# Optimization experiments

Hardware: AMD Instinct MI355X
Metric: run time of the kernel (lower is better)

Reference implementation:

```python
import jax, jax.numpy as jnp
import numpy as np

B, V, FN, C = 8, 50000, 100000, 64


def setup_inputs() -> dict:
    key = jax.random.key(0)
    keys = iter(jax.random.split(key, 16))
    inp = {}
    inp["centers"] = jax.random.normal(next(keys), (B, 3, FN), jnp.float32)
    inp["verts"] = jax.random.normal(next(keys), (B, V, 3), jnp.float32)
    inp["faces"] = jax.random.randint(next(keys), (B, FN, 3), 0, V)

    def bn(p):
        inp[p + "g"] = jnp.ones((C,), jnp.float32)
        inp[p + "bt"] = jnp.zeros((C,), jnp.float32)
        inp[p + "m"] = jnp.zeros((C,), jnp.float32)
        inp[p + "v"] = jnp.ones((C,), jnp.float32)

    inp["cw1"] = jax.random.normal(next(keys), (C, 3), jnp.float32) * 0.1
    inp["cb1"] = jnp.zeros((C,), jnp.float32); bn("c1")
    inp["cw2"] = jax.random.normal(next(keys), (C, C), jnp.float32) * 0.1
    inp["cb2"] = jnp.zeros((C,), jnp.float32); bn("c2")
    inp["vw1"] = jax.random.normal(next(keys), (C, 6), jnp.float32) * 0.1
    inp["vb1"] = jnp.zeros((C,), jnp.float32); bn("v1")
    inp["vw2"] = jax.random.normal(next(keys), (C, C), jnp.float32) * 0.1
    inp["vb2"] = jnp.zeros((C,), jnp.float32); bn("v2")
    inp["sw"] = jax.random.normal(next(keys), (C, 2 * C), jnp.float32) * 0.1
    inp["sb"] = jnp.zeros((C,), jnp.float32); bn("s1")
    return inp


def _cbr(x, w, b, g, bt, m, v, eps=1e-5):
    # 1x1 Conv1d == pointwise GEMM over channel dim, then eval-mode BN, then ReLU
    y = jnp.einsum('bcf,oc->bof', x, w) + b[:, None]
    y = (y - m[:, None]) * (g[:, None] / jnp.sqrt(v[:, None] + eps)) + bt[:, None]
    return jax.nn.relu(y)


def _forward(faces, centers, verts,
             cw1, cb1, c1g, c1bt, c1m, c1v, cw2, cb2, c2g, c2bt, c2m, c2v,
             vw1, vb1, v1g, v1bt, v1m, v1v, vw2, vb2, v2g, v2bt, v2m, v2v,
             sw, sb, s1g, s1bt, s1m, s1v):
    Bb, Fn, _ = faces.shape
    # gather 3 corner vertices per face: [B, 3F, 3] -> [B, 9, F] (v0xyz, v1xyz, v2xyz)
    idx = faces.reshape(Bb, Fn * 3)
    corners = jnp.take_along_axis(verts, idx[:, :, None], axis=1)
    c9 = corners.reshape(Bb, Fn, 9).transpose(0, 2, 1)

    def vmlp(x):
        return _cbr(_cbr(x, vw1, vb1, v1g, v1bt, v1m, v1v), vw2, vb2, v2g, v2bt, v2m, v2v)

    vfeat = (vmlp(c9[:, :6])
             + vmlp(c9[:, 3:9])
             + vmlp(jnp.concatenate([c9[:, 6:9], c9[:, :3]], axis=1))) / 3.0
    cfeat = _cbr(_cbr(centers, cw1, cb1, c1g, c1bt, c1m, c1v), cw2, cb2, c2g, c2bt, c2m, c2v)
    return _cbr(jnp.concatenate([cfeat, vfeat], axis=1), sw, sb, s1g, s1bt, s1m, s1v)


def reference(centers, verts, faces,
              cw1, cb1, c1g, c1bt, c1m, c1v, cw2, cb2, c2g, c2bt, c2m, c2v,
              vw1, vb1, v1g, v1bt, v1m, v1v, vw2, vb2, v2g, v2bt, v2m, v2v,
              sw, sb, s1g, s1bt, s1m, s1v):
    return _forward(faces, centers, verts,
                    cw1, cb1, c1g, c1bt, c1m, c1v, cw2, cb2, c2g, c2bt, c2m, c2v,
                    vw1, vb1, v1g, v1bt, v1m, v1v, vw2, vb2, v2g, v2bt, v2m, v2v,
                    sw, sb, s1g, s1bt, s1m, s1v)
```

## Files before the change

kernel.cpp:

```cpp
#include <hip/hip_runtime.h>
#include <cstddef>
#include <cstdint>

#define FN_ 100000
#define V_  50000
#define B_  8
#define NT  64
#define NBX ((FN_ + NT - 1) / NT)

#define WS_SHS 49152

typedef _Float16 f16;
typedef f16   f16x8 __attribute__((ext_vector_type(8)));
typedef float f32x4 __attribute__((ext_vector_type(4)));

struct Ptrs { const void* p[33]; };

union Pk8 { f16 h[8]; uint4 u; };

__device__ __forceinline__ uint32_t pack2(float a, float b) {
  return __builtin_bit_cast(uint32_t, __builtin_amdgcn_cvt_pkrtz(a, b));
}
__device__ __forceinline__ uint32_t pack_relu2(float a, float b) {
  uint32_t r, x = pack2(a, b);
  asm("v_pk_max_f16 %0, %1, 0" : "=v"(r) : "v"(x));
  return r;
}

__global__ __launch_bounds__(1024) void sd_prep(Ptrs in, f16* __restrict__ wsW,
                                                float* __restrict__ shsG)
{
  const float* __restrict__ cw1 = (const float*)in.p[3];
  const float* __restrict__ cb1 = (const float*)in.p[4];
  const float* __restrict__ c1g = (const float*)in.p[5];
  const float* __restrict__ c1bt= (const float*)in.p[6];
  const float* __restrict__ c1m = (const float*)in.p[7];
  const float* __restrict__ c1v = (const float*)in.p[8];
  const float* __restrict__ cw2 = (const float*)in.p[9];
  const float* __restrict__ cb2 = (const float*)in.p[10];
  const float* __restrict__ c2g = (const float*)in.p[11];
  const float* __restrict__ c2bt= (const float*)in.p[12];
  const float* __restrict__ c2m = (const float*)in.p[13];
  const float* __restrict__ c2v = (const float*)in.p[14];
  const float* __restrict__ vw1 = (const float*)in.p[15];
  const float* __restrict__ vb1 = (const float*)in.p[16];
  const float* __restrict__ v1g = (const float*)in.p[17];
  const float* __restrict__ v1bt= (const float*)in.p[18];
  const float* __restrict__ v1m = (const float*)in.p[19];
  const float* __restrict__ v1v = (const float*)in.p[20];
  const float* __restrict__ vw2 = (const float*)in.p[21];
  const float* __restrict__ vb2 = (const float*)in.p[22];
  const float* __restrict__ v2g = (const float*)in.p[23];
  const float* __restrict__ v2bt= (const float*)in.p[24];
  const float* __restrict__ v2m = (const float*)in.p[25];
  const float* __restrict__ v2v = (const float*)in.p[26];
  const float* __restrict__ sw  = (const float*)in.p[27];
  const float* __restrict__ sb  = (const float*)in.p[28];
  const float* __restrict__ s1g = (const float*)in.p[29];
  const float* __restrict__ s1bt= (const float*)in.p[30];
  const float* __restrict__ s1m = (const float*)in.p[31];
  const float* __restrict__ s1v = (const float*)in.p[32];

  __shared__ float scsL[448];
  const int tid = threadIdx.x;

  if (tid < 448) {
    const float *g, *v, *bb, *m, *bt; int o; float mul = 1.f;
    if (tid < 64)       { o = tid;      g=c1g; v=c1v; bb=cb1; m=c1m; bt=c1bt; }
    else if (tid < 256) { o = tid & 63; g=v1g; v=v1v; bb=vb1; m=v1m; bt=v1bt; }
    else if (tid < 320) { o = tid-256;  g=c2g; v=c2v; bb=cb2; m=c2m; bt=c2bt; }
    else if (tid < 384) { o = tid-320;  g=v2g; v=v2v; bb=vb2; m=v2m; bt=v2bt; mul = 1.f/3.f; }
    else                { o = tid-384;  g=s1g; v=s1v; bb=sb;  m=s1m; bt=s1bt; }
    float s = g[o] * rsqrtf(v[o] + 1e-5f);
    scsL[tid] = s * mul;
    shsG[tid] = ((bb[o] - m[o]) * s + bt[o]) * mul;
  }
  __syncthreads();

  for (int u = tid; u < 3072; u += 1024) {
    const int t = u >> 6, l = u & 63, r15 = l & 15, g4 = l >> 4;
    Pk8 pk;
    if (t < 16) {
      const int wm = t >> 2, tr = t & 3, row = 64*wm + 16*tr + r15;
#pragma unroll
      for (int j = 0; j < 8; ++j) {
        const int k = 8*g4 + j; float val = 0.f;
        if (wm == 0) { if (k >= 9 && k < 12) val = cw1[row*3 + (k-9)]; }
        else if (k < 9) {
          const int e = wm - 1, o = row - 64*wm, c = (k - 3*e + 9) % 9;
          if (c < 6) val = vw1[o*6 + c];
        }
        pk.h[j] = (f16)(val * scsL[row]);
      }
    } else if (t < 24) {
      const int tt = t-16, rt = tt >> 1, s = tt & 1, row = 16*rt + r15;
#pragma unroll
      for (int j = 0; j < 8; ++j) { const int k = 32*s + 8*g4 + j;
        pk.h[j] = (f16)(cw2[row*64 + k] * scsL[256+row]); }
    } else if (t < 32) {
      const int tt = t-24, rt = tt >> 1, s = tt & 1, row = 16*rt + r15;
#pragma unroll
      for (int j = 0; j < 8; ++j) { const int k = 32*s + 8*g4 + j;
        pk.h[j] = (f16)(vw2[row*64 + k] * scsL[320+row]); }
    } else {
      const int tt = t-32, rt = tt >> 2, s = tt & 3, row = 16*rt + r15;
#pragma unroll
      for (int j = 0; j < 8; ++j) { const int k = 32*s + 8*g4 + j;
        pk.h[j] = (f16)(sw[row*128 + k] * scsL[384+row]); }
    }
    *(uint4*)(wsW + (size_t)t*512 + l*8) = pk.u;
  }
}

__global__ __launch_bounds__(512, 8) void sd_main(const int* __restrict__ faces,
    const float* __restrict__ verts, const float* __restrict__ centers,
    const f16* __restrict__ wsW, const float* __restrict__ shsG,
    float* __restrict__ out)
{
  __shared__ f16 Hs[NT][296];
  __shared__ float shsL[448];

  const int tid  = threadIdx.x;
  const int lane = tid & 63;
  const int r15  = lane & 15;
  const int g4   = lane >> 4;
  const int w    = __builtin_amdgcn_readfirstlane(tid >> 6);
  const int by   = blockIdx.y;
  const int col0 = blockIdx.x * NT;

  if (tid < 448) shsL[tid] = shsG[tid];

  {
    const int col = tid >> 3, p = tid & 7;
    const int f = col0 + col;
    const bool valid = f < FN_;
    if (p < 3) {
      float x0 = 0.f, x1 = 0.f, x2 = 0.f;
      if (valid) {
        const int vi = faces[((size_t)by*FN_ + f)*3 + p];
        const float* vp = verts + ((size_t)by*V_ + (size_t)vi)*3;
        x0 = vp[0]; x1 = vp[1]; x2 = vp[2];
      }
      Hs[col][256 + p*3 + 0] = (f16)x0;
      Hs[col][256 + p*3 + 1] = (f16)x1;
      Hs[col][256 + p*3 + 2] = (f16)x2;
    } else if (p == 3) {
#pragma unroll
      for (int k = 0; k < 3; ++k)
        Hs[col][265 + k] = valid ? (f16)centers[((size_t)by*3 + k)*FN_ + f] : (f16)0.f;
    } else {
#pragma unroll
      for (int z = 0; z < 5; ++z) Hs[col][268 + (p-4)*5 + z] = (f16)0.f;
    }
  }
  __syncthreads();

  const f16* __restrict__ wfrag = wsW + lane*8;

  {
    const int t0 = 2*w, t1 = 2*w + 1;
    const f16x8 a0 = *(const f16x8*)(wfrag + (size_t)t0*512);
    const f16x8 a1 = *(const f16x8*)(wfrag + (size_t)t1*512);
    const f32x4 sh0 = *(const f32x4*)&shsL[t0*16 + 4*g4];
    const f32x4 sh1 = *(const f32x4*)&shsL[t1*16 + 4*g4];
#pragma unroll
    for (int tc = 0; tc < 4; ++tc) {
      const f16x8 b = *(const f16x8*)&Hs[16*tc + r15][256 + 8*g4];
      f32x4 c0 = __builtin_amdgcn_mfma_f32_16x16x32_f16(a0, b, sh0, 0,0,0);
      f32x4 c1 = __builtin_amdgcn_mfma_f32_16x16x32_f16(a1, b, sh1, 0,0,0);
      uint2 p0, p1;
      p0.x = pack_relu2(c0[0], c0[1]); p0.y = pack_relu2(c0[2], c0[3]);
      p1.x = pack_relu2(c1[0], c1[1]); p1.y = pack_relu2(c1[2], c1[3]);
      *(uint2*)&Hs[16*tc + r15][t0*16 + 4*g4] = p0;
      *(uint2*)&Hs[16*tc + r15][t1*16 + 4*g4] = p1;
    }
  }
  __syncthreads();

  const int rt = w & 3, cg = w >> 2;
  float cf[2][4], vf[2][4];

#pragma unroll
  for (int br = 0; br < 4; ++br) {
    const int wbase = br ? 24 : 16;
    const f16x8 a0 = *(const f16x8*)(wfrag + (size_t)(wbase + 2*rt + 0)*512);
    const f16x8 a1 = *(const f16x8*)(wfrag + (size_t)(wbase + 2*rt + 1)*512);
    const f32x4 shv = *(const f32x4*)&shsL[(br ? 320 : 256) + rt*16 + 4*g4];
#pragma unroll
    for (int tc = 0; tc < 2; ++tc) {
      const int col = 16*(2*cg + tc) + r15;
      const f16x8 b0 = *(const f16x8*)&Hs[col][64*br + 8*g4];
      const f16x8 b1 = *(const f16x8*)&Hs[col][64*br + 32 + 8*g4];
      f32x4 acc = __builtin_amdgcn_mfma_f32_16x16x32_f16(a0, b0, shv, 0,0,0);
      acc = __builtin_amdgcn_mfma_f32_16x16x32_f16(a1, b1, acc, 0,0,0);
#pragma unroll
      for (int j = 0; j < 4; ++j) {
        const float val = fmaxf(acc[j], 0.f);
        if (br == 0)      cf[tc][j]  = val;
        else if (br == 1) vf[tc][j]  = val;
        else              vf[tc][j] += val;
      }
    }
  }
  __syncthreads();

#pragma unroll
  for (int tc = 0; tc < 2; ++tc) {
    const int col = 16*(2*cg + tc) + r15;
    const int o0  = rt*16 + 4*g4;
    uint2 pc, pv;
    pc.x = pack2(cf[tc][0], cf[tc][1]); pc.y = pack2(cf[tc][2], cf[tc][3]);
    pv.x = pack2(vf[tc][0], vf[tc][1]); pv.y = pack2(vf[tc][2], vf[tc][3]);
    *(uint2*)&Hs[col][o0]      = pc;
    *(uint2*)&Hs[col][64 + o0] = pv;
  }
  __syncthreads();

  {
    const f32x4 shv = *(const f32x4*)&shsL[384 + rt*16 + 4*g4];
    f32x4 acc[2];
    acc[0] = shv; acc[1] = shv;
#pragma unroll
    for (int s = 0; s < 4; ++s) {
      const f16x8 a = *(const f16x8*)(wfrag + (size_t)(32 + rt*4 + s)*512);
#pragma unroll
      for (int tc = 0; tc < 2; ++tc) {
        const f16x8 b = *(const f16x8*)&Hs[16*(2*cg + tc) + r15][32*s + 8*g4];
        acc[tc] = __builtin_amdgcn_mfma_f32_16x16x32_f16(a, b, acc[tc], 0,0,0);
      }
    }
    const int o0 = rt*16 + 4*g4;
#pragma unroll
    for (int tc = 0; tc < 2; ++tc) {
      const int f = col0 + 16*(2*cg + tc) + r15;
      if (f < FN_) {
        const size_t base = ((size_t)(by*64 + o0))*FN_ + (size_t)f;
#pragma unroll
        for (int j = 0; j < 4; ++j)
          out[base + (size_t)j*FN_] = fmaxf(acc[tc][j], 0.f);
      }
    }
  }
}

extern "C" void kernel_launch(void* const* d_in, const int* in_sizes, int n_in,
                              void* d_out, int out_size, void* d_ws, size_t ws_size,
                              hipStream_t stream) {
  (void)in_sizes; (void)n_in; (void)out_size; (void)ws_size;
  Ptrs p;
  for (int i = 0; i < 33; ++i) p.p[i] = d_in[i];
  f16*   wsW  = (f16*)d_ws;
  float* shsG = (float*)((char*)d_ws + WS_SHS);
  hipLaunchKernelGGL(sd_prep, dim3(1), dim3(1024), 0, stream, p, wsW, shsG);
  hipLaunchKernelGGL(sd_main, dim3(NBX, B_), dim3(512), 0, stream,
                     (const int*)d_in[2], (const float*)d_in[1], (const float*)d_in[0],
                     wsW, shsG, (float*)d_out);
}
```

Before: 100.5 us.

## Make main kernel persistent with double-buffered gather overlapped with compute

Converts the main kernel from one block per 64-face tile into a persistent grid of 1024 blocks that loop over tiles. The gather of the next tile's vertex and center inputs is issued into a second LDS input slot while the current tile's second-layer MFMAs run. All weight fragments and BN shifts are hoisted into registers once per block, and the LDS tile is XOR-swizzled with a wider stride to cut bank conflicts. The costs are higher register pressure (launch bounds lowered to 4) and a fixed grid size that may leave load imbalance across CUs.

Measured after the change: 160.8 us. 60.1% more time.

```diff
diff --git a/kernel.cpp b/kernel.cpp
--- a/kernel.cpp
+++ b/kernel.cpp
@@ -7,6 +7,9 @@
 #define B_  8
 #define NT  64
 #define NBX ((FN_ + NT - 1) / NT)
+#define TT  (NBX * B_)
+#define GRIDX 1024
+#define STR 448
 
 #define WS_SHS 49152
 
@@ -112,28 +115,45 @@
   }
 }
 
-__global__ __launch_bounds__(512, 8) void sd_main(const int* __restrict__ faces,
+__global__ __launch_bounds__(512, 4) void sd_main(const int* __restrict__ faces,
     const float* __restrict__ verts, const float* __restrict__ centers,
     const f16* __restrict__ wsW, const float* __restrict__ shsG,
     float* __restrict__ out)
 {
-  __shared__ f16 Hs[NT][296];
-  __shared__ float shsL[448];
+  __shared__ __align__(16) f16 Hs[NT * STR];
 
   const int tid  = threadIdx.x;
   const int lane = tid & 63;
   const int r15  = lane & 15;
   const int g4   = lane >> 4;
   const int w    = __builtin_amdgcn_readfirstlane(tid >> 6);
-  const int by   = blockIdx.y;
-  const int col0 = blockIdx.x * NT;
-
-  if (tid < 448) shsL[tid] = shsG[tid];
-
-  {
+  const int SW   = (r15 & 7) << 3;
+  const int rt   = w & 3, cg = w >> 2;
+
+  const f16* wf = wsW + lane*8;
+  const f16x8 wL1a = *(const f16x8*)(wf + (size_t)(2*w    )*512);
+  const f16x8 wL1b = *(const f16x8*)(wf + (size_t)(2*w + 1)*512);
+  const f16x8 wC2a = *(const f16x8*)(wf + (size_t)(16 + 2*rt    )*512);
+  const f16x8 wC2b = *(const f16x8*)(wf + (size_t)(16 + 2*rt + 1)*512);
+  const f16x8 wV2a = *(const f16x8*)(wf + (size_t)(24 + 2*rt    )*512);
+  const f16x8 wV2b = *(const f16x8*)(wf + (size_t)(24 + 2*rt + 1)*512);
+  f16x8 wS[4];
+#pragma unroll
+  for (int s = 0; s < 4; ++s)
+    wS[s] = *(const f16x8*)(wf + (size_t)(32 + 4*rt + s)*512);
+  const f32x4 shL1a = *(const f32x4*)&shsG[(2*w    )*16 + 4*g4];
+  const f32x4 shL1b = *(const f32x4*)&shsG[(2*w + 1)*16 + 4*g4];
+  const f32x4 shC2  = *(const f32x4*)&shsG[256 + rt*16 + 4*g4];
+  const f32x4 shV2  = *(const f32x4*)&shsG[320 + rt*16 + 4*g4];
+  const f32x4 shS   = *(const f32x4*)&shsG[384 + rt*16 + 4*g4];
+
+  auto gather = [&](int tile, int xk) {
     const int col = tid >> 3, p = tid & 7;
-    const int f = col0 + col;
+    const int by = tile / NBX, bx = tile - by*NBX;
+    const int f = bx*NT + col;
     const bool valid = f < FN_;
+    const int swg = (col & 7) << 3;
+    f16* xp = &Hs[col*STR];
     if (p < 3) {
       float x0 = 0.f, x1 = 0.f, x2 = 0.f;
       if (valid) {
@@ -141,105 +161,124 @@
         const float* vp = verts + ((size_t)by*V_ + (size_t)vi)*3;
         x0 = vp[0]; x1 = vp[1]; x2 = vp[2];
       }
-      Hs[col][256 + p*3 + 0] = (f16)x0;
-      Hs[col][256 + p*3 + 1] = (f16)x1;
-      Hs[col][256 + p*3 + 2] = (f16)x2;
+      const int k0 = xk + p*3;
+      xp[(k0+0) ^ swg] = (f16)x0;
+      xp[(k0+1) ^ swg] = (f16)x1;
+      xp[(k0+2) ^ swg] = (f16)x2;
     } else if (p == 3) {
 #pragma unroll
       for (int k = 0; k < 3; ++k)
-        Hs[col][265 + k] = valid ? (f16)centers[((size_t)by*3 + k)*FN_ + f] : (f16)0.f;
-    } else {
-#pragma unroll
-      for (int z = 0; z < 5; ++z) Hs[col][268 + (p-4)*5 + z] = (f16)0.f;
-    }
-  }
-  __syncthreads();
-
-  const f16* __restrict__ wfrag = wsW + lane*8;
-
-  {
-    const int t0 = 2*w, t1 = 2*w + 1;
-    const f16x8 a0 = *(const f16x8*)(wfrag + (size_t)t0*512);
-    const f16x8 a1 = *(const f16x8*)(wfrag + (size_t)t1*512);
-    const f32x4 sh0 = *(const f32x4*)&shsL[t0*16 + 4*g4];
-    const f32x4 sh1 = *(const f32x4*)&shsL[t1*16 + 4*g4];
+        xp[(xk+9+k) ^ swg] = valid ? (f16)centers[((size_t)by*3 + k)*FN_ + f] : (f16)0.f;
+    }
+  };
+
+  auto runL1 = [&](int xk) {
+    const int t0k = (2*w)*16 + 4*g4;
+    const int t1k = t0k + 16;
 #pragma unroll
     for (int tc = 0; tc < 4; ++tc) {
-      const f16x8 b = *(const f16x8*)&Hs[16*tc + r15][256 + 8*g4];
-      f32x4 c0 = __builtin_amdgcn_mfma_f32_16x16x32_f16(a0, b, sh0, 0,0,0);
-      f32x4 c1 = __builtin_amdgcn_mfma_f32_16x16x32_f16(a1, b, sh1, 0,0,0);
+      const int colo = (16*tc + r15) * STR;
+      const f16x8 b = *(const f16x8*)&Hs[colo + ((xk + 8*g4) ^ SW)];
+      f32x4 c0 = __builtin_amdgcn_mfma_f32_16x16x32_f16(wL1a, b, shL1a, 0,0,0);
+      f32x4 c1 = __builtin_amdgcn_mfma_f32_16x16x32_f16(wL1b, b, shL1b, 0,0,0);
       uint2 p0, p1;
       p0.x = pack_relu2(c0[0], c0[1]); p0.y = pack_relu2(c0[2], c0[3]);
       p1.x = pack_relu2(c1[0], c1[1]); p1.y = pack_relu2(c1[2], c1[3]);
-      *(uint2*)&Hs[16*tc + r15][t0*16 + 4*g4] = p0;
-      *(uint2*)&Hs[16*tc + r15][t1*16 + 4*g4] = p1;
-    }
-  }
+      *(uint2*)&Hs[colo + (t0k ^ SW)] = p0;
+      *(uint2*)&Hs[colo + (t1k ^ SW)] = p1;
+    }
+  };
+
+  {
+    const int col = tid >> 3, p = tid & 7;
+    const int swg = (col & 7) << 3;
+    f16* xp = &Hs[col*STR];
+#pragma unroll
+    for (int z = 0; z < 5; ++z) {
+      const int zz = p*5 + z;
+      const int k = (zz < 20) ? (384 + 12 + zz) : (416 + 12 + (zz - 20));
+      xp[k ^ swg] = (f16)0.f;
+    }
+  }
+  int tile = blockIdx.x;
+  gather(tile, 384);
   __syncthreads();
-
-  const int rt = w & 3, cg = w >> 2;
-  float cf[2][4], vf[2][4];
-
-#pragma unroll
-  for (int br = 0; br < 4; ++br) {
-    const int wbase = br ? 24 : 16;
-    const f16x8 a0 = *(const f16x8*)(wfrag + (size_t)(wbase + 2*rt + 0)*512);
-    const f16x8 a1 = *(const f16x8*)(wfrag + (size_t)(wbase + 2*rt + 1)*512);
-    const f32x4 shv = *(const f32x4*)&shsL[(br ? 320 : 256) + rt*16 + 4*g4];
+  runL1(384);
+  __syncthreads();
+
+  int cur = 0;
+#pragma unroll 1
+  for (;;) {
+    const int nxt = tile + GRIDX;
+    const bool hasNext = nxt < TT;
+    const int xkNext = 384 + 32*(cur ^ 1);
+
+    float cf[2][4], vf[2][4];
+#pragma unroll
+    for (int br = 0; br < 4; ++br) {
+      const f16x8 a0 = br ? wV2a : wC2a;
+      const f16x8 a1 = br ? wV2b : wC2b;
+      const f32x4 shv = br ? shV2 : shC2;
+#pragma unroll
+      for (int tc = 0; tc < 2; ++tc) {
+        const int colo = (16*(2*cg + tc) + r15) * STR;
+        const f16x8 b0 = *(const f16x8*)&Hs[colo + ((64*br +      8*g4) ^ SW)];
+        const f16x8 b1 = *(const f16x8*)&Hs[colo + ((64*br + 32 + 8*g4) ^ SW)];
+        f32x4 acc = __builtin_amdgcn_mfma_f32_16x16x32_f16(a0, b0, shv, 0,0,0);
+        acc = __builtin_amdgcn_mfma_f32_16x16x32_f16(a1, b1, acc, 0,0,0);
+#pragma unroll
+        for (int j = 0; j < 4; ++j) {
+          const float val = fmaxf(acc[j], 0.f);
+          if (br == 0)      cf[tc][j]  = val;
+          else if (br == 1) vf[tc][j]  = val;
+          else              vf[tc][j] += val;
+        }
+      }
+    }
+    if (hasNext) gather(nxt, xkNext);
+    __syncthreads();
+
 #pragma unroll
     for (int tc = 0; tc < 2; ++tc) {
-      const int col = 16*(2*cg + tc) + r15;
-      const f16x8 b0 = *(const f16x8*)&Hs[col][64*br + 8*g4];
-      const f16x8 b1 = *(const f16x8*)&Hs[col][64*br + 32 + 8*g4];
-      f32x4 acc = __builtin_amdgcn_mfma_f32_16x16x32_f16(a0, b0, shv, 0,0,0);
-      acc = __builtin_amdgcn_mfma_f32_16x16x32_f16(a1, b1, acc, 0,0,0);
-#pragma unroll
-      for (int j = 0; j < 4; ++j) {
-        const float val = fmaxf(acc[j], 0.f);
-        if (br == 0)      cf[tc][j]  = val;
-        else if (br == 1) vf[tc][j]  = val;
-        else              vf[tc][j] += val;
-      }
-    }
-  }
-  __syncthreads();
-
-#pragma unroll
-  for (int tc = 0; tc < 2; ++tc) {
-    const int col = 16*(2*cg + tc) + r15;
-    const int o0  = rt*16 + 4*g4;
-    uint2 pc, pv;
-    pc.x = pack2(cf[tc][0], cf[tc][1]); pc.y = pack2(cf[tc][2], cf[tc][3]);
-    pv.x = pack2(vf[tc][0], vf[tc][1]); pv.y = pack2(vf[tc][2], vf[tc][3]);
-    *(uint2*)&Hs[col][o0]      = pc;
-    *(uint2*)&Hs[col][64 + o0] = pv;
-  }
-  __syncthreads();
-
-  {
-    const f32x4 shv = *(const f32x4*)&shsL[384 + rt*16 + 4*g4];
-    f32x4 acc[2];
-    acc[0] = shv; acc[1] = shv;
-#pragma unroll
-    for (int s = 0; s < 4; ++s) {
-      const f16x8 a = *(const f16x8*)(wfrag + (size_t)(32 + rt*4 + s)*512);
+      const int colo = (16*(2*cg + tc) + r15) * STR;
+      const int o0 = rt*16 + 4*g4;
+      uint2 pc, pv;
+      pc.x = pack2(cf[tc][0], cf[tc][1]); pc.y = pack2(cf[tc][2], cf[tc][3]);
+      pv.x = pack2(vf[tc][0], vf[tc][1]); pv.y = pack2(vf[tc][2], vf[tc][3]);
+      *(uint2*)&Hs[colo + ((256 + o0) ^ SW)]      = pc;
+      *(uint2*)&Hs[colo + ((256 + 64 + o0) ^ SW)] = pv;
+    }
+    __syncthreads();
+
+    {
+      f32x4 acc[2];
+      acc[0] = shS; acc[1] = shS;
+#pragma unroll
+      for (int s = 0; s < 4; ++s) {
+#pragma unroll
+        for (int tc = 0; tc < 2; ++tc) {
+          const int colo = (16*(2*cg + tc) + r15) * STR;
+          const f16x8 b = *(const f16x8*)&Hs[colo + ((256 + 32*s + 8*g4) ^ SW)];
+          acc[tc] = __builtin_amdgcn_mfma_f32_16x16x32_f16(wS[s], b, acc[tc], 0,0,0);
+        }
+      }
+      const int by = tile / NBX, bx = tile - by*NBX;
+      const int o0 = rt*16 + 4*g4;
 #pragma unroll
       for (int tc = 0; tc < 2; ++tc) {
-        const f16x8 b = *(const f16x8*)&Hs[16*(2*cg + tc) + r15][32*s + 8*g4];
-        acc[tc] = __builtin_amdgcn_mfma_f32_16x16x32_f16(a, b, acc[tc], 0,0,0);
-      }
-    }
-    const int o0 = rt*16 + 4*g4;
-#pragma unroll
-    for (int tc = 0; tc < 2; ++tc) {
-      const int f = col0 + 16*(2*cg + tc) + r15;
-      if (f < FN_) {
-        const size_t base = ((size_t)(by*64 + o0))*FN_ + (size_t)f;
-#pragma unroll
-        for (int j = 0; j < 4; ++j)
-          out[base + (size_t)j*FN_] = fmaxf(acc[tc][j], 0.f);
-      }
-    }
+        const int f = bx*NT + 16*(2*cg + tc) + r15;
+        if (f < FN_) {
+          const size_t base = ((size_t)(by*64 + o0))*FN_ + (size_t)f;
+#pragma unroll
+          for (int j = 0; j < 4; ++j)
+            out[base + (size_t)j*FN_] = fmaxf(acc[tc][j], 0.f);
+        }
+      }
+    }
+    if (!hasNext) break;
+    runL1(xkNext);
+    __syncthreads();
+    tile = nxt; cur ^= 1;
   }
 }
 
@@ -252,7 +291,7 @@
   f16*   wsW  = (f16*)d_ws;
   float* shsG = (float*)((char*)d_ws + WS_SHS);
   hipLaunchKernelGGL(sd_prep, dim3(1), dim3(1024), 0, stream, p, wsW, shsG);
-  hipLaunchKernelGGL(sd_main, dim3(NBX, B_), dim3(512), 0, stream,
+  hipLaunchKernelGGL(sd_main, dim3(GRIDX), dim3(512), 0, stream,
                      (const int*)d_in[2], (const float*)d_in[1], (const float*)d_in[0],
                      wsW, shsG, (float*)d_out);
 }
```
